# Optimization experiments

Hardware: AMD Instinct MI355X
Metric: run time of the kernel (lower is better)

Reference implementation:

```python
import jax, jax.numpy as jnp
import numpy as np

N_NODES = 120000
EM = 128
N_EDGES = 1920000
BS = 1024
L = 10

def setup_inputs() -> dict:
    key = jax.random.key(0)
    ks = jax.random.split(key, 24)
    stdv = 1.0 / np.sqrt(EM)
    u = lambda k, shape: jax.random.uniform(k, shape, jnp.float32, -stdv, stdv)
    return {
        'src': jax.random.randint(ks[0], (N_EDGES,), 0, N_NODES, jnp.int32),
        'dst': jax.random.randint(ks[1], (N_EDGES,), 0, N_NODES, jnp.int32),
        'user': jax.random.randint(ks[2], (BS, 1), 0, 20000, jnp.int32),
        'seq': jax.random.randint(ks[3], (BS, L), 0, 100000, jnp.int32),
        'mask': jnp.ones((BS, L), jnp.float32),
        'seq_len': jax.random.randint(ks[4], (BS,), 1, L, jnp.int32),
        'pos_idx': jax.random.randint(ks[5], (BS, L), 0, 200, jnp.int32),
        'item_num': 100000,
        'v2e': u(ks[6], (N_NODES, EM)),
        'W_self': u(ks[7], (EM, EM)),
        'W_neigh': u(ks[8], (EM, EM)),
        'sage_b': u(ks[9], (EM,)),
        'pos_emb': u(ks[10], (200, EM)),
        'w1': u(ks[11], (2 * EM, EM)),
        'w2': u(ks[12], (EM, 1)),
        'glu1_w': u(ks[13], (EM, EM)),
        'glu1_b': u(ks[14], (EM,)),
        'glu2_w': u(ks[15], (EM, EM)),
        'w3': u(ks[16], (EM, EM)),
        'w4': u(ks[17], (EM, 1)),
        'glu3_w': u(ks[18], (EM, EM)),
        'glu3_b': u(ks[19], (EM,)),
        'glu4_w': u(ks[20], (EM, EM)),
        'sc_w': u(ks[21], (2 * EM, 1)),
        'sc_b': u(ks[22], (1,)),
    }


def reference(src, dst, user, seq, mask, seq_len, pos_idx, item_num,
              v2e, W_self, W_neigh, sage_b, pos_emb,
              w1, w2, glu1_w, glu1_b, glu2_w,
              w3, w4, glu3_w, glu3_b, glu4_w, sc_w, sc_b):
    N = v2e.shape[0]
    # SAGEConv 'mean': fc_self(x) + fc_neigh(mean over in-neighbors) + bias, then ReLU
    deg = jax.ops.segment_sum(jnp.ones_like(dst, jnp.float32), dst, num_segments=N)
    agg = jax.ops.segment_sum(v2e[src], dst, num_segments=N)
    agg = agg / jnp.clip(deg, 1.0)[:, None]
    h1 = jax.nn.relu(v2e @ W_self + agg @ W_neigh + sage_b)

    u_idx = user + item_num                      # [bs,1]
    node_embeds = (h1[seq] + v2e[seq]) * 0.5     # [bs,L,em]
    user_embeds = (h1[u_idx] + v2e[u_idx]) * 0.5 # [bs,1,em]
    seq_embeds = user_embeds[:, 0]               # [bs,em]

    m = mask[..., None]                          # [bs,L,1]
    # compute_hidden_vector (GLU-gated attention with positional embedding)
    pe = pos_emb[pos_idx]                        # [bs,L,em]
    tmp = jnp.sum(node_embeds * m, axis=1) / jnp.sum(m, axis=1)  # masked mean [bs,em]
    hs = tmp[:, None, :]
    nh = jnp.tanh(jnp.concatenate([pe, node_embeds], -1) @ w1)
    nh = jax.nn.sigmoid(nh @ glu1_w + glu1_b + hs @ glu2_w)
    beta = (nh @ w2) * m
    sess_vec = jnp.sum(beta * node_embeds, axis=1)  # [bs,em]

    # sess_user_vector
    nh2 = jnp.tanh(node_embeds @ w3)
    nh2 = jax.nn.sigmoid(nh2 @ glu3_w + glu3_b + user_embeds @ glu4_w)
    beta2 = (nh2 @ w4) * m
    sess_user = jnp.sum(beta2 * node_embeds, axis=1)  # [bs,em]

    alpha = jax.nn.sigmoid(jnp.concatenate([sess_vec, sess_user], 1) @ sc_w + sc_b)  # [bs,1]
    seq_embeds = seq_embeds + alpha * sess_vec + (1.0 - alpha) * sess_user

    scores = seq_embeds @ v2e[1:].T              # [bs, N-1]
    return scores
```

## Files before the change

### kernel.cpp

```cpp
#include <hip/hip_runtime.h>
#include <stdint.h>

#define N_NODES   120000
#define EM        128
#define N_EDGES_C 1920000
#define BSZ       1024
#define SL        10
#define N_GATHER  (BSZ*SL + BSZ)
#define N_OUTCOL  (N_NODES - 1)
#define NBLK_E    1875
#define CHUNK_E   1024
#define NPANEL    938
#define NBLK_S    (NPANEL*8)

typedef __attribute__((ext_vector_type(8))) short bf16x8;
typedef __attribute__((ext_vector_type(4))) float f32x4;

#define GLOBAL_AS __attribute__((address_space(1)))
#define LDS_AS    __attribute__((address_space(3)))

__device__ inline void gload_lds16(const void* g, void* l) {
  __builtin_amdgcn_global_load_lds((const GLOBAL_AS unsigned int*)g,
                                   (LDS_AS unsigned int*)l, 16, 0, 0);
}

__device__ inline unsigned pk_bf16(float a, float b) {
  unsigned ua = __builtin_bit_cast(unsigned, a);
  ua += 0x7fffu + ((ua >> 16) & 1u);
  unsigned ub = __builtin_bit_cast(unsigned, b);
  ub += 0x7fffu + ((ub >> 16) & 1u);
  return (ua >> 16) | (ub & 0xffff0000u);
}

#define MAP_OFF   0u
#define CNT_OFF   480000u
#define DEG_OFF   480256u
#define OFFS_OFF  525312u
#define CUR_OFF   570368u
#define AGG_OFF   615424u
#define EPAIR_OFF 6382592u
#define SORT_OFF  21742592u
#define BCNT_OFF  (SORT_OFF + 6291456u)
#define BOFF_OFF  (BCNT_OFF + 8192u)
#define NE_OFF    29422592u
#define UE_OFF    34665472u
#define SB_OFF    35189760u
#define V2EB_OFF  37748736u

__global__ __launch_bounds__(256) void k_tobf16(const float* __restrict__ v2e,
    unsigned short* __restrict__ v2eb) {
  size_t base = ((size_t)blockIdx.x*256 + threadIdx.x) * 8;
  float4 v0 = *(const float4*)(v2e + base);
  float4 v1 = *(const float4*)(v2e + base + 4);
  uint4 o;
  o.x = pk_bf16(v0.x, v0.y); o.y = pk_bf16(v0.z, v0.w);
  o.z = pk_bf16(v1.x, v1.y); o.w = pk_bf16(v1.z, v1.w);
  *(uint4*)(v2eb + base) = o;
}

__global__ __launch_bounds__(256) void k_assign(const int* __restrict__ seq,
    const int* __restrict__ user, const int* __restrict__ item_num,
    int* __restrict__ map, int* __restrict__ slotCount) {
  int t = blockIdx.x*256 + threadIdx.x;
  int idx = (t < BSZ*SL) ? seq[t] : (user[t - BSZ*SL] + item_num[0]);
  int old = atomicCAS(map + idx, -1, -2);
  if (old == -1) {
    int slot = atomicAdd(slotCount, 1);
    atomicExch(map + idx, slot);
  }
}

__global__ __launch_bounds__(256) void k_count(const int* __restrict__ src,
    const int* __restrict__ dst, const int* __restrict__ map,
    int* __restrict__ blockCnt, int* __restrict__ deg_i) {
  __shared__ int wsum[4];
  int tid = threadIdx.x, lane = tid & 63, wv = tid >> 6;
  int beg = blockIdx.x * CHUNK_E;
  int local = 0;
  #pragma unroll
  for (int it = 0; it < CHUNK_E/256; ++it) {
    int e = beg + it*256 + tid;
    int slot = map[dst[e]];
    bool flag = slot >= 0;
    if (flag) atomicAdd(deg_i + slot, 1);
    unsigned long long m = __ballot(flag);
    if (lane == 0) local += __popcll(m);
  }
  if (lane == 0) wsum[wv] = local;
  __syncthreads();
  if (tid == 0) blockCnt[blockIdx.x] = wsum[0] + wsum[1] + wsum[2] + wsum[3];
}

__global__ __launch_bounds__(256) void k_scanblk(const int* __restrict__ blockCnt,
    int* __restrict__ blockOffs, int* __restrict__ ecount) {
  __shared__ int wsum[4];
  int tid = threadIdx.x, lane = tid & 63, wv = tid >> 6;
  int carry = 0;
  for (int c = 0; c < 8; ++c) {
    int i = c*256 + tid;
    int v = (i < NBLK_E) ? blockCnt[i] : 0;
    int s = v;
    #pragma unroll
    for (int o = 1; o < 64; o <<= 1) {
      int t = __shfl_up(s, o);
      if (lane >= o) s += t;
    }
    if (lane == 63) wsum[wv] = s;
    __syncthreads();
    int wbase = 0, tot = 0;
    #pragma unroll
    for (int q = 0; q < 4; ++q) { int vq = wsum[q]; if (q < wv) wbase += vq; tot += vq; }
    if (i < NBLK_E) blockOffs[i] = s - v + wbase + carry;
    carry += tot;
    __syncthreads();
  }
  if (tid == 0) ecount[0] = carry;
}

__global__ __launch_bounds__(256) void k_place(const int* __restrict__ src,
    const int* __restrict__ dst, const int* __restrict__ map,
    const int* __restrict__ blockOffs, int* __restrict__ epairs) {
  __shared__ int wsum[4];
  int tid = threadIdx.x, lane = tid & 63, wv = tid >> 6;
  int beg = blockIdx.x * CHUNK_E;
  int base = blockOffs[blockIdx.x];
  int carry = 0;
  #pragma unroll
  for (int it = 0; it < CHUNK_E/256; ++it) {
    int e = beg + it*256 + tid;
    int s = src[e];
    int slot = map[dst[e]];
    bool flag = slot >= 0;
    unsigned long long m = __ballot(flag);
    if (lane == 0) wsum[wv] = __popcll(m);
    __syncthreads();
    int wbase = 0, tot = 0;
    #pragma unroll
    for (int q = 0; q < 4; ++q) { int vq = wsum[q]; if (q < wv) wbase += vq; tot += vq; }
    if (flag) {
      int pos = base + carry + wbase + __popcll(m & ((1ull << lane) - 1ull));
      epairs[2*pos]   = s;
      epairs[2*pos+1] = slot;
    }
    carry += tot;
    __syncthreads();
  }
}

__global__ __launch_bounds__(256) void k_scan(const int* __restrict__ deg_i,
    int* __restrict__ offs, int* __restrict__ cursor) {
  __shared__ int wsum[4];
  int tid = threadIdx.x;
  int lane = tid & 63, wv = tid >> 6;
  int carry = 0;
  for (int c = 0; c < N_GATHER/256; ++c) {
    int i = c*256 + tid;
    int v = deg_i[i];
    int s = v;
    #pragma unroll
    for (int o = 1; o < 64; o <<= 1) {
      int t = __shfl_up(s, o);
      if (lane >= o) s += t;
    }
    if (lane == 63) wsum[wv] = s;
    __syncthreads();
    int wbase = 0;
    #pragma unroll
    for (int q = 0; q < 4; ++q) if (q < wv) wbase += wsum[q];
    int tot = wsum[0] + wsum[1] + wsum[2] + wsum[3];
    int excl = s - v + wbase + carry;
    offs[i] = excl;
    cursor[i] = excl;
    carry += tot;
    __syncthreads();
  }
}

__global__ __launch_bounds__(256) void k_scatter(const int* __restrict__ epairs,
    const int* __restrict__ ecount, int* __restrict__ cursor, int* __restrict__ sorted) {
  int E = ecount[0];
  int T = gridDim.x*blockDim.x;
  for (int e = blockIdx.x*blockDim.x + threadIdx.x; e < E; e += T) {
    int s = epairs[2*e], slot = epairs[2*e+1];
    int pos = atomicAdd(cursor + slot, 1);
    sorted[pos] = s;
  }
}

__global__ __launch_bounds__(256) void k_reduce(const float* __restrict__ v2e,
    const int* __restrict__ offs, const int* __restrict__ deg_i,
    const int* __restrict__ slotCount, const int* __restrict__ sorted,
    float* __restrict__ agg) {
  int nslots = slotCount[0];
  int g = (blockIdx.x*blockDim.x + threadIdx.x) >> 5;
  int lg = threadIdx.x & 31;
  int ngrp = (gridDim.x*blockDim.x) >> 5;
  for (int slot = g; slot < nslots; slot += ngrp) {
    int beg = offs[slot];
    int end = beg + deg_i[slot];
    float4 a = make_float4(0.f, 0.f, 0.f, 0.f);
    for (int e = beg; e < end; ++e) {
      int s = sorted[e];
      const float4 v = *(const float4*)(v2e + (size_t)s*EM + lg*4);
      a.x += v.x; a.y += v.y; a.z += v.z; a.w += v.w;
    }
    *(float4*)(agg + (size_t)slot*EM + lg*4) = a;
  }
}

__global__ __launch_bounds__(128) void k_embed(const int* __restrict__ seq,
    const int* __restrict__ user, const int* __restrict__ item_num,
    const int* __restrict__ map, const int* __restrict__ deg_i,
    const float* __restrict__ agg, const float* __restrict__ v2e,
    const float* __restrict__ W_self, const float* __restrict__ W_neigh,
    const float* __restrict__ sage_b,
    float* __restrict__ node_emb, float* __restrict__ user_emb) {
  __shared__ float xs[8][EM];
  __shared__ float xa[8][EM];
  int j = threadIdx.x;
  int base = blockIdx.x * 8;
  #pragma unroll
  for (int r = 0; r < 8; ++r) {
    int rg = base + r;
    int idx = (rg < BSZ*SL) ? seq[rg] : (user[rg - BSZ*SL] + item_num[0]);
    int slot = map[idx];
    float rd = 1.0f / fmaxf((float)deg_i[slot], 1.0f);
    xs[r][j] = v2e[(size_t)idx*EM + j];
    xa[r][j] = agg[(size_t)slot*EM + j] * rd;
  }
  __syncthreads();
  float acc[8] = {0.f,0.f,0.f,0.f,0.f,0.f,0.f,0.f};
  for (int k = 0; k < EM; ++k) {
    float a  = W_self[k*EM + j];
    float bb = W_neigh[k*EM + j];
    #pragma unroll
    for (int r = 0; r < 8; ++r) acc[r] += xs[r][k]*a + xa[r][k]*bb;
  }
  float bias = sage_b[j];
  #pragma unroll
  for (int r = 0; r < 8; ++r) {
    int rg = base + r;
    float h = fmaxf(acc[r] + bias, 0.0f);
    float emb = 0.5f * (h + xs[r][j]);
    if (rg < BSZ*SL) node_emb[(size_t)rg*EM + j] = emb;
    else             user_emb[(size_t)(rg - BSZ*SL)*EM + j] = emb;
  }
}

__global__ __launch_bounds__(128) void k_session(
    const float* __restrict__ node_emb, const float* __restrict__ user_emb,
    const int* __restrict__ pos_idx, const float* __restrict__ mask_in,
    const float* __restrict__ pos_emb,
    const float* __restrict__ w1, const float* __restrict__ w2,
    const float* __restrict__ glu1_w, const float* __restrict__ glu1_b,
    const float* __restrict__ glu2_w,
    const float* __restrict__ w3, const float* __restrict__ w4,
    const float* __restrict__ glu3_w, const float* __restrict__ glu3_b,
    const float* __restrict__ glu4_w,
    const float* __restrict__ sc_w, const float* __restrict__ sc_b,
    unsigned short* __restrict__ seqb) {
  __shared__ float ne[SL][EM], pe[SL][EM], r1[SL][EM], r2[SL][EM];
  __shared__ float ue[EM], hsS[EM], redA[EM];
  __shared__ float mls[SL], bl1[SL], bl2[SL];
  __shared__ float alphaS;
  int b = blockIdx.x, j = threadIdx.x;
  ue[j] = user_emb[b*EM + j];
  if (j < SL) mls[j] = mask_in[b*SL + j];
  #pragma unroll
  for (int l = 0; l < SL; ++l) {
    ne[l][j] = node_emb[(size_t)(b*SL + l)*EM + j];
    int p = pos_idx[b*SL + l];
    pe[l][j] = pos_emb[(size_t)p*EM + j];
  }
  __syncthreads();
  float s = 0.f, ms = 0.f;
  #pragma unroll
  for (int l = 0; l < SL; ++l) { s += mls[l]*ne[l][j]; ms += mls[l]; }
  hsS[j] = s / ms;
  float a1[SL], a2[SL];
  #pragma unroll
  for (int l = 0; l < SL; ++l) { a1[l] = 0.f; a2[l] = 0.f; }
  for (int k = 0; k < EM; ++k) {
    float wt  = w1[k*EM + j];
    float wb  = w1[(k+EM)*EM + j];
    float w3v = w3[k*EM + j];
    #pragma unroll
    for (int l = 0; l < SL; ++l) {
      a1[l] += pe[l][k]*wt + ne[l][k]*wb;
      a2[l] += ne[l][k]*w3v;
    }
  }
  #pragma unroll
  for (int l = 0; l < SL; ++l) { r1[l][j] = tanhf(a1[l]); r2[l][j] = tanhf(a2[l]); }
  __syncthreads();
  float g1[SL], g2[SL];
  #pragma unroll
  for (int l = 0; l < SL; ++l) { g1[l] = 0.f; g2[l] = 0.f; }
  float hsa = 0.f, uea = 0.f;
  for (int k = 0; k < EM; ++k) {
    float c1 = glu1_w[k*EM + j];
    float c2 = glu2_w[k*EM + j];
    float c3 = glu3_w[k*EM + j];
    float c4 = glu4_w[k*EM + j];
    hsa += hsS[k]*c2;
    uea += ue[k]*c4;
    #pragma unroll
    for (int l = 0; l < SL; ++l) {
      g1[l] += r1[l][k]*c1;
      g2[l] += r2[l][k]*c3;
    }
  }
  float b1 = glu1_b[j], b3 = glu3_b[j];
  float w2v = w2[j], w4v = w4[j];
  __syncthreads();
  #pragma unroll
  for (int l = 0; l < SL; ++l) {
    float s1 = 1.f/(1.f + expf(-(g1[l] + b1 + hsa)));
    float s2 = 1.f/(1.f + expf(-(g2[l] + b3 + uea)));
    r1[l][j] = s1 * w2v;
    r2[l][j] = s2 * w4v;
  }
  __syncthreads();
  if (j < SL) {
    float t1 = 0.f, t2 = 0.f;
    for (int t = 0; t < EM; ++t) { t1 += r1[j][t]; t2 += r2[j][t]; }
    bl1[j] = t1 * mls[j];
    bl2[j] = t2 * mls[j];
  }
  __syncthreads();
  float sv = 0.f, su = 0.f;
  #pragma unroll
  for (int l = 0; l < SL; ++l) { sv += bl1[l]*ne[l][j]; su += bl2[l]*ne[l][j]; }
  redA[j] = sv*sc_w[j] + su*sc_w[EM + j];
  __syncthreads();
  if (j == 0) {
    float t = 0.f;
    for (int k = 0; k < EM; ++k) t += redA[k];
    alphaS = 1.f/(1.f + expf(-(t + sc_b[0])));
  }
  __syncthreads();
  float al = alphaS;
  float val = ue[j] + al*sv + (1.f - al)*su;
  unsigned uv = __builtin_bit_cast(unsigned, val);
  uv += 0x7fffu + ((uv >> 16) & 1u);
  seqb[b*EM + j] = (unsigned short)(uv >> 16);
}

__global__ __launch_bounds__(256, 3) void k_scores(
    const unsigned short* __restrict__ seqb,
    const unsigned short* __restrict__ v2eb, float* __restrict__ out) {
  __shared__ char Bs[32768];
  __shared__ float scr[4][16][68];
  int tid = threadIdx.x;
  int bid = blockIdx.x;
  int lid = (bid & 7) * (NBLK_S/8) + (bid >> 3);
  int m0 = (lid & 7) * 128;
  int n0 = (lid >> 3) * 128;
  int w = tid >> 6, lane = tid & 63;
  const char* v2eb_c = (const char*)v2eb;
  #pragma unroll
  for (int i = 0; i < 8; ++i) {
    int chunk = i*4 + w;
    int o = chunk*1024 + lane*16;
    int row = o >> 8;
    int c = o & 255;
    int rowg = n0 + 1 + row;
    if (rowg > N_OUTCOL) rowg = N_OUTCOL;
    const void* src = v2eb_c + (size_t)rowg*256 + (c ^ ((row & 7) << 4));
    gload_lds16(src, Bs + chunk*1024);
  }
  asm volatile("s_waitcnt vmcnt(0)");
  __syncthreads();

  int wm = w >> 1, wn = w & 1;
  int lr = lane & 15, lg = lane >> 4;
  f32x4 acc[4][4];
  #pragma unroll
  for (int mi = 0; mi < 4; ++mi)
    #pragma unroll
    for (int ni = 0; ni < 4; ++ni)
      acc[mi][ni] = 0.f;
  #pragma unroll
  for (int ks = 0; ks < 4; ++ks) {
    bf16x8 a[4], bfr[4];
    #pragma unroll
    for (int mi = 0; mi < 4; ++mi)
      a[mi] = *(const bf16x8*)(seqb + (size_t)(m0 + wm*64 + mi*16 + lr)*EM + ks*32 + lg*8);
    #pragma unroll
    for (int ni = 0; ni < 4; ++ni) {
      int row = wn*64 + ni*16 + lr;
      int off = (row*256 + ks*64 + lg*16) ^ ((row & 7) << 4);
      bfr[ni] = *(const bf16x8*)(Bs + off);
    }
    #pragma unroll
    for (int mi = 0; mi < 4; ++mi)
      #pragma unroll
      for (int ni = 0; ni < 4; ++ni)
        acc[mi][ni] = __builtin_amdgcn_mfma_f32_16x16x32_bf16(a[mi], bfr[ni], acc[mi][ni], 0, 0, 0);
  }

  float (*sw)[68] = scr[w];
  int nbase = n0 + wn*64;
  #pragma unroll
  for (int mi = 0; mi < 4; ++mi) {
    #pragma unroll
    for (int ni = 0; ni < 4; ++ni)
      #pragma unroll
      for (int r = 0; r < 4; ++r)
        sw[lg*4 + r][ni*16 + lr] = acc[mi][ni][r];
    asm volatile("s_waitcnt lgkmcnt(0)" ::: "memory");
    #pragma unroll
    for (int q = 0; q < 4; ++q) {
      int row16 = q*4 + lg;
      float4 v = *(const float4*)&sw[row16][lr*4];
      int m = m0 + wm*64 + mi*16 + row16;
      int nc = nbase + lr*4;
      size_t base = (size_t)m * N_OUTCOL + nc;
      if (nc + 3 < N_OUTCOL) {
        *(float4*)(out + base) = v;
      } else if (nc < N_OUTCOL) {
        float vv[4] = {v.x, v.y, v.z, v.w};
        #pragma unroll
        for (int t = 0; t < 4; ++t)
          if (nc + t < N_OUTCOL) out[base + t] = vv[t];
      }
    }
    asm volatile("s_waitcnt lgkmcnt(0)" ::: "memory");
  }
}

extern "C" void kernel_launch(void* const* d_in, const int* in_sizes, int n_in,
                              void* d_out, int out_size, void* d_ws, size_t ws_size,
                              hipStream_t stream) {
  const int*   src      = (const int*)d_in[0];
  const int*   dst      = (const int*)d_in[1];
  const int*   user     = (const int*)d_in[2];
  const int*   seq      = (const int*)d_in[3];
  const float* mask     = (const float*)d_in[4];
  const int*   pos_idx  = (const int*)d_in[6];
  const int*   item_num = (const int*)d_in[7];
  const float* v2e      = (const float*)d_in[8];
  const float* W_self   = (const float*)d_in[9];
  const float* W_neigh  = (const float*)d_in[10];
  const float* sage_b   = (const float*)d_in[11];
  const float* pos_emb  = (const float*)d_in[12];
  const float* w1       = (const float*)d_in[13];
  const float* w2       = (const float*)d_in[14];
  const float* glu1_w   = (const float*)d_in[15];
  const float* glu1_b   = (const float*)d_in[16];
  const float* glu2_w   = (const float*)d_in[17];
  const float* w3       = (const float*)d_in[18];
  const float* w4       = (const float*)d_in[19];
  const float* glu3_w   = (const float*)d_in[20];
  const float* glu3_b   = (const float*)d_in[21];
  const float* glu4_w   = (const float*)d_in[22];
  const float* sc_w     = (const float*)d_in[23];
  const float* sc_b     = (const float*)d_in[24];
  float* out = (float*)d_out;
  char*  ws  = (char*)d_ws;

  int*   map       = (int*)(ws + MAP_OFF);
  int*   slotCount = (int*)(ws + CNT_OFF);
  int*   ecount    = slotCount + 1;
  int*   deg_i     = (int*)(ws + DEG_OFF);
  int*   offs      = (int*)(ws + OFFS_OFF);
  int*   cursor    = (int*)(ws + CUR_OFF);
  float* agg       = (float*)(ws + AGG_OFF);
  int*   epairs    = (int*)(ws + EPAIR_OFF);
  int*   sorted    = (int*)(ws + SORT_OFF);
  int*   blockCnt  = (int*)(ws + BCNT_OFF);
  int*   blockOffs = (int*)(ws + BOFF_OFF);
  float* node_emb  = (float*)(ws + NE_OFF);
  float* user_emb  = (float*)(ws + UE_OFF);
  unsigned short* seqb  = (unsigned short*)(ws + SB_OFF);
  unsigned short* v2eb  = (unsigned short*)(ws + V2EB_OFF);

  hipMemsetAsync(map, 0xFF, 480000, stream);
  hipMemsetAsync(ws + CNT_OFF, 0, (DEG_OFF - CNT_OFF) + 45056, stream);
  k_tobf16<<<7500, 256, 0, stream>>>(v2e, v2eb);
  k_assign<<<N_GATHER/256, 256, 0, stream>>>(seq, user, item_num, map, slotCount);
  k_count<<<NBLK_E, 256, 0, stream>>>(src, dst, map, blockCnt, deg_i);
  k_scanblk<<<1, 256, 0, stream>>>(blockCnt, blockOffs, ecount);
  k_place<<<NBLK_E, 256, 0, stream>>>(src, dst, map, blockOffs, epairs);
  k_scan<<<1, 256, 0, stream>>>(deg_i, offs, cursor);
  k_scatter<<<1024, 256, 0, stream>>>(epairs, ecount, cursor, sorted);
  k_reduce<<<1408, 256, 0, stream>>>(v2e, offs, deg_i, slotCount, sorted, agg);
  k_embed<<<N_GATHER/8, 128, 0, stream>>>(seq, user, item_num, map, deg_i, agg, v2e,
                                          W_self, W_neigh, sage_b, node_emb, user_emb);
  k_session<<<BSZ, 128, 0, stream>>>(node_emb, user_emb, pos_idx, mask, pos_emb,
      w1, w2, glu1_w, glu1_b, glu2_w, w3, w4, glu3_w, glu3_b, glu4_w, sc_w, sc_b, seqb);
  k_scores<<<NBLK_S, 256, 0, stream>>>(seqb, v2eb, out);
}
```

Measured before the change: 421.8 us.

## Fuse edge placement into atomic scatter, gather bf16 neighbors, replace memsets

Drops the block-count scan, compacted edge-pair buffer and separate scatter pass. Edges are placed directly into per-slot sorted lists with atomic cursors after the degree scan. The neighbor aggregation now gathers bf16 copies of v2e, halving gather traffic at some precision cost in the aggregated sum. Two memsets become a single init kernel.

```diff
diff --git a/kernel.cpp b/kernel.cpp
--- a/kernel.cpp
+++ b/kernel.cpp
@@ -32,20 +32,26 @@
   return (ua >> 16) | (ub & 0xffff0000u);
 }
 
+__device__ inline float bf2f(unsigned short u) {
+  return __builtin_bit_cast(float, ((unsigned)u) << 16);
+}
+
 #define MAP_OFF   0u
 #define CNT_OFF   480000u
 #define DEG_OFF   480256u
 #define OFFS_OFF  525312u
 #define CUR_OFF   570368u
 #define AGG_OFF   615424u
-#define EPAIR_OFF 6382592u
 #define SORT_OFF  21742592u
-#define BCNT_OFF  (SORT_OFF + 6291456u)
-#define BOFF_OFF  (BCNT_OFF + 8192u)
 #define NE_OFF    29422592u
 #define UE_OFF    34665472u
 #define SB_OFF    35189760u
 #define V2EB_OFF  37748736u
+
+__global__ __launch_bounds__(256) void k_init(int* __restrict__ ws_ints) {
+  int t = blockIdx.x*256 + threadIdx.x;
+  ws_ints[t] = (t < N_NODES) ? -1 : 0;
+}
 
 __global__ __launch_bounds__(256) void k_tobf16(const float* __restrict__ v2e,
     unsigned short* __restrict__ v2eb) {
@@ -70,80 +76,14 @@
   }
 }
 
-__global__ __launch_bounds__(256) void k_count(const int* __restrict__ src,
-    const int* __restrict__ dst, const int* __restrict__ map,
-    int* __restrict__ blockCnt, int* __restrict__ deg_i) {
-  __shared__ int wsum[4];
-  int tid = threadIdx.x, lane = tid & 63, wv = tid >> 6;
+__global__ __launch_bounds__(256) void k_count(const int* __restrict__ dst,
+    const int* __restrict__ map, int* __restrict__ deg_i) {
   int beg = blockIdx.x * CHUNK_E;
-  int local = 0;
   #pragma unroll
   for (int it = 0; it < CHUNK_E/256; ++it) {
-    int e = beg + it*256 + tid;
+    int e = beg + it*256 + threadIdx.x;
     int slot = map[dst[e]];
-    bool flag = slot >= 0;
-    if (flag) atomicAdd(deg_i + slot, 1);
-    unsigned long long m = __ballot(flag);
-    if (lane == 0) local += __popcll(m);
-  }
-  if (lane == 0) wsum[wv] = local;
-  __syncthreads();
-  if (tid == 0) blockCnt[blockIdx.x] = wsum[0] + wsum[1] + wsum[2] + wsum[3];
-}
-
-__global__ __launch_bounds__(256) void k_scanblk(const int* __restrict__ blockCnt,
-    int* __restrict__ blockOffs, int* __restrict__ ecount) {
-  __shared__ int wsum[4];
-  int tid = threadIdx.x, lane = tid & 63, wv = tid >> 6;
-  int carry = 0;
-  for (int c = 0; c < 8; ++c) {
-    int i = c*256 + tid;
-    int v = (i < NBLK_E) ? blockCnt[i] : 0;
-    int s = v;
-    #pragma unroll
-    for (int o = 1; o < 64; o <<= 1) {
-      int t = __shfl_up(s, o);
-      if (lane >= o) s += t;
-    }
-    if (lane == 63) wsum[wv] = s;
-    __syncthreads();
-    int wbase = 0, tot = 0;
-    #pragma unroll
-    for (int q = 0; q < 4; ++q) { int vq = wsum[q]; if (q < wv) wbase += vq; tot += vq; }
-    if (i < NBLK_E) blockOffs[i] = s - v + wbase + carry;
-    carry += tot;
-    __syncthreads();
-  }
-  if (tid == 0) ecount[0] = carry;
-}
-
-__global__ __launch_bounds__(256) void k_place(const int* __restrict__ src,
-    const int* __restrict__ dst, const int* __restrict__ map,
-    const int* __restrict__ blockOffs, int* __restrict__ epairs) {
-  __shared__ int wsum[4];
-  int tid = threadIdx.x, lane = tid & 63, wv = tid >> 6;
-  int beg = blockIdx.x * CHUNK_E;
-  int base = blockOffs[blockIdx.x];
-  int carry = 0;
-  #pragma unroll
-  for (int it = 0; it < CHUNK_E/256; ++it) {
-    int e = beg + it*256 + tid;
-    int s = src[e];
-    int slot = map[dst[e]];
-    bool flag = slot >= 0;
-    unsigned long long m = __ballot(flag);
-    if (lane == 0) wsum[wv] = __popcll(m);
-    __syncthreads();
-    int wbase = 0, tot = 0;
-    #pragma unroll
-    for (int q = 0; q < 4; ++q) { int vq = wsum[q]; if (q < wv) wbase += vq; tot += vq; }
-    if (flag) {
-      int pos = base + carry + wbase + __popcll(m & ((1ull << lane) - 1ull));
-      epairs[2*pos]   = s;
-      epairs[2*pos+1] = slot;
-    }
-    carry += tot;
-    __syncthreads();
+    if (slot >= 0) atomicAdd(deg_i + slot, 1);
   }
 }
 
@@ -176,18 +116,22 @@
   }
 }
 
-__global__ __launch_bounds__(256) void k_scatter(const int* __restrict__ epairs,
-    const int* __restrict__ ecount, int* __restrict__ cursor, int* __restrict__ sorted) {
-  int E = ecount[0];
-  int T = gridDim.x*blockDim.x;
-  for (int e = blockIdx.x*blockDim.x + threadIdx.x; e < E; e += T) {
-    int s = epairs[2*e], slot = epairs[2*e+1];
-    int pos = atomicAdd(cursor + slot, 1);
-    sorted[pos] = s;
-  }
-}
-
-__global__ __launch_bounds__(256) void k_reduce(const float* __restrict__ v2e,
+__global__ __launch_bounds__(256) void k_place(const int* __restrict__ src,
+    const int* __restrict__ dst, const int* __restrict__ map,
+    int* __restrict__ cursor, int* __restrict__ sorted) {
+  int beg = blockIdx.x * CHUNK_E;
+  #pragma unroll
+  for (int it = 0; it < CHUNK_E/256; ++it) {
+    int e = beg + it*256 + threadIdx.x;
+    int slot = map[dst[e]];
+    if (slot >= 0) {
+      int pos = atomicAdd(cursor + slot, 1);
+      sorted[pos] = src[e];
+    }
+  }
+}
+
+__global__ __launch_bounds__(256) void k_reduce(const unsigned short* __restrict__ v2eb,
     const int* __restrict__ offs, const int* __restrict__ deg_i,
     const int* __restrict__ slotCount, const int* __restrict__ sorted,
     float* __restrict__ agg) {
@@ -198,13 +142,13 @@
   for (int slot = g; slot < nslots; slot += ngrp) {
     int beg = offs[slot];
     int end = beg + deg_i[slot];
-    float4 a = make_float4(0.f, 0.f, 0.f, 0.f);
+    float a0 = 0.f, a1 = 0.f, a2 = 0.f, a3 = 0.f;
     for (int e = beg; e < end; ++e) {
       int s = sorted[e];
-      const float4 v = *(const float4*)(v2e + (size_t)s*EM + lg*4);
-      a.x += v.x; a.y += v.y; a.z += v.z; a.w += v.w;
-    }
-    *(float4*)(agg + (size_t)slot*EM + lg*4) = a;
+      ushort4 v = *(const ushort4*)(v2eb + (size_t)s*EM + lg*4);
+      a0 += bf2f(v.x); a1 += bf2f(v.y); a2 += bf2f(v.z); a3 += bf2f(v.w);
+    }
+    *(float4*)(agg + (size_t)slot*EM + lg*4) = make_float4(a0, a1, a2, a3);
   }
 }
 
@@ -461,30 +405,23 @@
 
   int*   map       = (int*)(ws + MAP_OFF);
   int*   slotCount = (int*)(ws + CNT_OFF);
-  int*   ecount    = slotCount + 1;
   int*   deg_i     = (int*)(ws + DEG_OFF);
   int*   offs      = (int*)(ws + OFFS_OFF);
   int*   cursor    = (int*)(ws + CUR_OFF);
   float* agg       = (float*)(ws + AGG_OFF);
-  int*   epairs    = (int*)(ws + EPAIR_OFF);
   int*   sorted    = (int*)(ws + SORT_OFF);
-  int*   blockCnt  = (int*)(ws + BCNT_OFF);
-  int*   blockOffs = (int*)(ws + BOFF_OFF);
   float* node_emb  = (float*)(ws + NE_OFF);
   float* user_emb  = (float*)(ws + UE_OFF);
   unsigned short* seqb  = (unsigned short*)(ws + SB_OFF);
   unsigned short* v2eb  = (unsigned short*)(ws + V2EB_OFF);
 
-  hipMemsetAsync(map, 0xFF, 480000, stream);
-  hipMemsetAsync(ws + CNT_OFF, 0, (DEG_OFF - CNT_OFF) + 45056, stream);
+  k_init<<<513, 256, 0, stream>>>((int*)ws);
   k_tobf16<<<7500, 256, 0, stream>>>(v2e, v2eb);
   k_assign<<<N_GATHER/256, 256, 0, stream>>>(seq, user, item_num, map, slotCount);
-  k_count<<<NBLK_E, 256, 0, stream>>>(src, dst, map, blockCnt, deg_i);
-  k_scanblk<<<1, 256, 0, stream>>>(blockCnt, blockOffs, ecount);
-  k_place<<<NBLK_E, 256, 0, stream>>>(src, dst, map, blockOffs, epairs);
+  k_count<<<NBLK_E, 256, 0, stream>>>(dst, map, deg_i);
   k_scan<<<1, 256, 0, stream>>>(deg_i, offs, cursor);
-  k_scatter<<<1024, 256, 0, stream>>>(epairs, ecount, cursor, sorted);
-  k_reduce<<<1408, 256, 0, stream>>>(v2e, offs, deg_i, slotCount, sorted, agg);
+  k_place<<<NBLK_E, 256, 0, stream>>>(src, dst, map, cursor, sorted);
+  k_reduce<<<1408, 256, 0, stream>>>(v2eb, offs, deg_i, slotCount, sorted, agg);
   k_embed<<<N_GATHER/8, 128, 0, stream>>>(seq, user, item_num, map, deg_i, agg, v2e,
                                           W_self, W_neigh, sage_b, node_emb, user_emb);
   k_session<<<BSZ, 128, 0, stream>>>(node_emb, user_emb, pos_idx, mask, pos_emb,
```

Result: faster. 398.6 us (-5.5%).
